# Kernel optimization log

Measured on AMD Instinct MI355X. Metric: run time of the kernel, lower is better.

The kernel has to match this reference:

```python
import jax, jax.numpy as jnp
import numpy as np

NUM_CLUSTERS = 16
CHANNELS = 256
UPDATE_RATE = 0.2
# channels % num_clusters == 0 -> all cluster capacities equal
_BASE = CHANNELS // NUM_CLUSTERS
_REM = CHANNELS % NUM_CLUSTERS
CLUSTER_SIZES = jnp.asarray([_BASE + 1] * _REM + [_BASE] * (NUM_CLUSTERS - _REM), dtype=jnp.int32)


def _cdist(a, b):
    # euclidean pairwise distance, batched over leading dims
    d2 = (jnp.sum(a * a, -1)[..., :, None]
          + jnp.sum(b * b, -1)[..., None, :]
          - 2.0 * (a @ jnp.swapaxes(b, -1, -2)))
    return jnp.sqrt(jnp.clip(d2, 0.0))


def _fps(D, k):
    # farthest point sampling given full [N,N] distance matrix
    start = jnp.argmax(D.sum(1))
    def step(min_d, _):
        far = jnp.argmax(min_d)
        return jnp.minimum(min_d, D[far]), far
    _, rest = jax.lax.scan(step, D[start], None, length=k - 1)
    return jnp.concatenate([start[None], rest])


def _capacity_assign(D, sizes):
    # greedy fixed-capacity assignment, sequential over channels
    order = jnp.argsort(D, axis=1)  # [C, K] cluster preference per channel
    def step(counts, row):
        avail = counts[row] < sizes[row]
        chosen = row[jnp.argmax(avail)]  # first available preference
        return counts.at[chosen].add(1), chosen
    _, assign = jax.lax.scan(step, jnp.zeros(sizes.shape[0], jnp.int32), order)
    return assign


def setup_inputs() -> dict:
    key = jax.random.key(0)
    k1, k2 = jax.random.split(key)
    features = jax.random.normal(k1, (8, CHANNELS, 64, 256), dtype=jnp.float32)
    pos_emb_batch = jax.random.normal(k2, (8, CHANNELS, 3), dtype=jnp.float32)
    return {"features": features, "pos_emb_batch": pos_emb_batch}


def reference(features, pos_emb_batch):
    b, c, nw, df = features.shape
    K = NUM_CLUSTERS
    pos = pos_emb_batch[0]                                   # [C, 3] (module's pos_emb buffer)
    # _initialize_centers: FPS over electrode positions
    centers = pos[_fps(_cdist(pos, pos), K)]                 # [K, 3]
    # _find_farthest_channels (euclidean): FPS over flattened features per batch
    ff = features.reshape(b, c, -1)
    Db = _cdist(ff, ff)                                      # [b, C, C]
    sel = jax.vmap(lambda D: _fps(D, K))(Db)                 # [b, K]
    # _cluster_euclidean_temp: nearest temp center per channel
    center_coords = pos_emb_batch[jnp.arange(b)[:, None], sel]      # [b, K, 3]
    temp_assign = jnp.argmin(_cdist(pos_emb_batch, center_coords), -1)  # [b, C]
    # per-cluster mean of positions over the whole batch
    flat_a = temp_assign.reshape(-1)
    flat_p = pos_emb_batch.reshape(-1, 3)
    sums = jax.ops.segment_sum(flat_p, flat_a, num_segments=K)
    cnts = jax.ops.segment_sum(jnp.ones(flat_a.shape, jnp.float32), flat_a, num_segments=K)
    avg = jnp.where(cnts[:, None] > 0, sums / jnp.maximum(cnts, 1.0)[:, None], 0.0)
    # match old centers to batch-average temp centers and EMA update
    matching = jnp.argmin(_cdist(centers, avg), axis=1)
    centers = (1.0 - UPDATE_RATE) * centers + UPDATE_RATE * avg[matching]
    # capacity-constrained final assignment
    return _capacity_assign(_cdist(pos, centers), CLUSTER_SIZES)
```

## Files before the change

kernel.cpp:

```cpp
#include <hip/hip_runtime.h>

#define NB 8
#define NC 256
#define DF 16384
#define KCL 16
#define SPLITS 8
#define KC (DF / SPLITS)
#define BK 32
#define ITERS (KC / BK)
#define NTILE 10

typedef _Float16 half8 __attribute__((ext_vector_type(8)));
typedef float floatx4 __attribute__((ext_vector_type(4)));

__device__ const int TItab[NTILE] = {0,0,0,0,1,1,1,2,2,3};
__device__ const int TJtab[NTILE] = {0,1,2,3,1,2,3,2,3,3};

__device__ __forceinline__ int argmax256(float v, float* sv, int* si) {
  int t = threadIdx.x;
  sv[t] = v; si[t] = t;
  __syncthreads();
  #pragma unroll
  for (int s = 128; s >= 1; s >>= 1) {
    if (t < s) {
      float a = sv[t], b = sv[t + s];
      int ia = si[t], ib = si[t + s];
      if (b > a || (b == a && ib < ia)) { sv[t] = b; si[t] = ib; }
    }
    __syncthreads();
  }
  int r = si[0];
  __syncthreads();
  return r;
}

__global__ __launch_bounds__(256) void k_pos_fps(const float* __restrict__ pe,
                                                 float* __restrict__ Dpos,
                                                 float* __restrict__ centers0) {
  __shared__ float px[NC], py[NC], pz[NC], pn[NC];
  __shared__ float sv[NC]; __shared__ int si[NC];
  __shared__ int fpsIdx[KCL];
  int t = threadIdx.x;
  float x = pe[t * 3 + 0], y = pe[t * 3 + 1], z = pe[t * 3 + 2];
  px[t] = x; py[t] = y; pz[t] = z;
  float n = x * x + y * y + z * z;
  pn[t] = n;
  __syncthreads();
  float rs = 0.f;
  for (int j = 0; j < NC; ++j) {
    float dot = x * px[j] + y * py[j] + z * pz[j];
    float d2 = n + pn[j] - 2.f * dot;
    float d = sqrtf(fmaxf(d2, 0.f));
    Dpos[j * NC + t] = d;
    rs += d;
  }
  __syncthreads();
  int start = argmax256(rs, sv, si);
  if (t == 0) fpsIdx[0] = start;
  float mind = Dpos[start * NC + t];
  for (int it = 1; it < KCL; ++it) {
    int far = argmax256(mind, sv, si);
    if (t == 0) fpsIdx[it] = far;
    mind = fminf(mind, Dpos[far * NC + t]);
  }
  __syncthreads();
  if (t < KCL) {
    int p = fpsIdx[t];
    centers0[t * 3 + 0] = px[p];
    centers0[t * 3 + 1] = py[p];
    centers0[t * 3 + 2] = pz[p];
  }
}

__global__ __launch_bounds__(256, 3) void k_gemm_mfma(const float* __restrict__ ff,
                                                      float* __restrict__ Pp) {
  __shared__ _Float16 Ah[64][40];
  __shared__ _Float16 Al[64][40];
  __shared__ _Float16 Bh[64][40];
  __shared__ _Float16 Bl[64][40];

  const int tid = threadIdx.x;
  const int tp = blockIdx.x;
  const int ti = TItab[tp], tj = TJtab[tp];
  const bool diag = (ti == tj);
  const int b = blockIdx.y, sp = blockIdx.z;
  const int wave = tid >> 6, lane = tid & 63;
  const int lrow = lane & 15, q = lane >> 4;

  const int sr = tid >> 2;
  const int sc = (tid & 3) * 8;
  const float* gA = ff + ((size_t)(b * NC + ti * 64 + sr)) * DF + sp * KC + sc;
  const float* gB = ff + ((size_t)(b * NC + tj * 64 + sr)) * DF + sp * KC + sc;

  floatx4 a1[4], a2[4], a3[4];
  #pragma unroll
  for (int j = 0; j < 4; ++j) { a1[j] = (floatx4)0.f; a2[j] = (floatx4)0.f; a3[j] = (floatx4)0.f; }

  float4 ra0 = *(const float4*)(gA), ra1 = *(const float4*)(gA + 4);
  float4 rb0 = make_float4(0.f, 0.f, 0.f, 0.f), rb1 = rb0;
  if (!diag) { rb0 = *(const float4*)(gB); rb1 = *(const float4*)(gB + 4); }
  gA += BK; gB += BK;

  for (int it = 0; it < ITERS; ++it) {
    float fa[8] = {ra0.x, ra0.y, ra0.z, ra0.w, ra1.x, ra1.y, ra1.z, ra1.w};
    half8 ah, al;
    #pragma unroll
    for (int e = 0; e < 8; ++e) {
      _Float16 h = (_Float16)fa[e];
      ah[e] = h;
      al[e] = (_Float16)(fa[e] - (float)h);
    }
    half8 bh, bl;
    if (!diag) {
      float fb[8] = {rb0.x, rb0.y, rb0.z, rb0.w, rb1.x, rb1.y, rb1.z, rb1.w};
      #pragma unroll
      for (int e = 0; e < 8; ++e) {
        _Float16 h = (_Float16)fb[e];
        bh[e] = h;
        bl[e] = (_Float16)(fb[e] - (float)h);
      }
    }
    __syncthreads();
    *(half8*)&Ah[sr][sc] = ah;
    *(half8*)&Al[sr][sc] = al;
    if (!diag) {
      *(half8*)&Bh[sr][sc] = bh;
      *(half8*)&Bl[sr][sc] = bl;
    }
    __syncthreads();
    if (it + 1 < ITERS) {
      ra0 = *(const float4*)(gA); ra1 = *(const float4*)(gA + 4);
      if (!diag) { rb0 = *(const float4*)(gB); rb1 = *(const float4*)(gB + 4); }
      gA += BK; gB += BK;
    }
    const _Float16* bhp = diag ? &Ah[0][0] : &Bh[0][0];
    const _Float16* blp = diag ? &Al[0][0] : &Bl[0][0];
    half8 af = *(const half8*)&Ah[wave * 16 + lrow][q * 8];
    half8 lf = *(const half8*)&Al[wave * 16 + lrow][q * 8];
    #pragma unroll
    for (int j = 0; j < 4; ++j) {
      half8 bhf = *(const half8*)(bhp + (j * 16 + lrow) * 40 + q * 8);
      half8 blf = *(const half8*)(blp + (j * 16 + lrow) * 40 + q * 8);
      a1[j] = __builtin_amdgcn_mfma_f32_16x16x32_f16(af, bhf, a1[j], 0, 0, 0);
      a2[j] = __builtin_amdgcn_mfma_f32_16x16x32_f16(af, blf, a2[j], 0, 0, 0);
      a3[j] = __builtin_amdgcn_mfma_f32_16x16x32_f16(lf, bhf, a3[j], 0, 0, 0);
    }
  }

  float* Pb = Pp + (size_t)(sp * NB + b) * NC * NC;
  int grow = ti * 64 + wave * 16 + q * 4;
  #pragma unroll
  for (int j = 0; j < 4; ++j) {
    int gcol = tj * 64 + j * 16 + lrow;
    float4 v;
    v.x = a1[j][0] + a2[j][0] + a3[j][0];
    v.y = a1[j][1] + a2[j][1] + a3[j][1];
    v.z = a1[j][2] + a2[j][2] + a3[j][2];
    v.w = a1[j][3] + a2[j][3] + a3[j][3];
    Pb[(size_t)(grow + 0) * NC + gcol] = v.x;
    Pb[(size_t)(grow + 1) * NC + gcol] = v.y;
    Pb[(size_t)(grow + 2) * NC + gcol] = v.z;
    Pb[(size_t)(grow + 3) * NC + gcol] = v.w;
    if (!diag) *(float4*)&Pb[(size_t)gcol * NC + grow] = v;
  }
}

__global__ __launch_bounds__(256) void k_diag(const float* __restrict__ Pp,
                                              float* __restrict__ dg) {
  int b = blockIdx.x, t = threadIdx.x;
  float s = 0.f;
  #pragma unroll
  for (int sp = 0; sp < SPLITS; ++sp)
    s += Pp[((size_t)(sp * NB + b) * NC + t) * NC + t];
  dg[b * NC + t] = s;
}

__global__ __launch_bounds__(256) void k_formD(const float* __restrict__ Pp,
                                               const float* __restrict__ dg,
                                               float* __restrict__ Db) {
  int i = blockIdx.x, b = blockIdx.y, j = threadIdx.x;
  float acc = 0.f;
  #pragma unroll
  for (int sp = 0; sp < SPLITS; ++sp)
    acc += Pp[((size_t)(sp * NB + b) * NC + i) * NC + j];
  float d2 = dg[b * NC + i] + dg[b * NC + j] - 2.f * acc;
  Db[((size_t)b * NC + i) * NC + j] = sqrtf(fmaxf(d2, 0.f));
}

__global__ __launch_bounds__(256) void k_fps_b(const float* __restrict__ Db,
                                               const float* __restrict__ pe,
                                               int* __restrict__ sel,
                                               float* __restrict__ ccoord) {
  int b = blockIdx.x, t = threadIdx.x;
  const float* D = Db + (size_t)b * NC * NC;
  __shared__ float sv[NC]; __shared__ int si[NC];
  __shared__ int fpsIdx[KCL];
  float rs = 0.f;
  for (int i = 0; i < NC; ++i) rs += D[i * NC + t];
  int start = argmax256(rs, sv, si);
  if (t == 0) fpsIdx[0] = start;
  float mind = D[start * NC + t];
  for (int it = 1; it < KCL; ++it) {
    int far = argmax256(mind, sv, si);
    if (t == 0) fpsIdx[it] = far;
    mind = fminf(mind, D[far * NC + t]);
  }
  __syncthreads();
  if (t < KCL) {
    int p = fpsIdx[t];
    sel[b * KCL + t] = p;
    ccoord[(b * KCL + t) * 3 + 0] = pe[(b * NC + p) * 3 + 0];
    ccoord[(b * KCL + t) * 3 + 1] = pe[(b * NC + p) * 3 + 1];
    ccoord[(b * KCL + t) * 3 + 2] = pe[(b * NC + p) * 3 + 2];
  }
}

__global__ __launch_bounds__(256) void k_final(const float* __restrict__ pe,
                                               const float* __restrict__ ccoord,
                                               const float* __restrict__ centers0,
                                               int* __restrict__ outp) {
  __shared__ float cc[NB * KCL * 3];
  __shared__ float cn[NB * KCL];
  __shared__ float sums[KCL][3];
  __shared__ int cnts[KCL];
  __shared__ float avg[KCL][3];
  __shared__ float an[KCL];
  __shared__ float c0[KCL * 3];
  __shared__ float c1x[KCL], c1y[KCL], c1z[KCL], c1n[KCL];
  __shared__ int order[NC][KCL];
  int t = threadIdx.x;
  for (int i = t; i < NB * KCL * 3; i += 256) cc[i] = ccoord[i];
  if (t < KCL * 3) c0[t] = centers0[t];
  if (t < KCL) { sums[t][0] = 0.f; sums[t][1] = 0.f; sums[t][2] = 0.f; cnts[t] = 0; }
  __syncthreads();
  if (t < NB * KCL) {
    float x = cc[t * 3], y = cc[t * 3 + 1], z = cc[t * 3 + 2];
    cn[t] = x * x + y * y + z * z;
  }
  __syncthreads();
  for (int b = 0; b < NB; ++b) {
    int p = b * NC + t;
    float x = pe[p * 3], y = pe[p * 3 + 1], z = pe[p * 3 + 2];
    float n = x * x + y * y + z * z;
    float best = 3.4e38f; int bi = 0;
    #pragma unroll
    for (int k = 0; k < KCL; ++k) {
      int c = b * KCL + k;
      float dot = x * cc[c * 3] + y * cc[c * 3 + 1] + z * cc[c * 3 + 2];
      float d2 = fmaxf(n + cn[c] - 2.f * dot, 0.f);
      if (d2 < best) { best = d2; bi = k; }
    }
    atomicAdd(&sums[bi][0], x);
    atomicAdd(&sums[bi][1], y);
    atomicAdd(&sums[bi][2], z);
    atomicAdd(&cnts[bi], 1);
  }
  __syncthreads();
  if (t < KCL) {
    float c = (float)cnts[t];
    float inv = 1.f / fmaxf(c, 1.f);
    float ax = (cnts[t] > 0) ? sums[t][0] * inv : 0.f;
    float ay = (cnts[t] > 0) ? sums[t][1] * inv : 0.f;
    float az = (cnts[t] > 0) ? sums[t][2] * inv : 0.f;
    avg[t][0] = ax; avg[t][1] = ay; avg[t][2] = az;
    an[t] = ax * ax + ay * ay + az * az;
  }
  __syncthreads();
  if (t < KCL) {
    float x = c0[t * 3], y = c0[t * 3 + 1], z = c0[t * 3 + 2];
    float n = x * x + y * y + z * z;
    float best = 3.4e38f; int bi = 0;
    #pragma unroll
    for (int j = 0; j < KCL; ++j) {
      float dot = x * avg[j][0] + y * avg[j][1] + z * avg[j][2];
      float d2 = fmaxf(n + an[j] - 2.f * dot, 0.f);
      if (d2 < best) { best = d2; bi = j; }
    }
    float nx = 0.8f * x + 0.2f * avg[bi][0];
    float ny = 0.8f * y + 0.2f * avg[bi][1];
    float nz = 0.8f * z + 0.2f * avg[bi][2];
    c1x[t] = nx; c1y[t] = ny; c1z[t] = nz;
    c1n[t] = nx * nx + ny * ny + nz * nz;
  }
  __syncthreads();
  {
    float x = pe[t * 3], y = pe[t * 3 + 1], z = pe[t * 3 + 2];
    float n = x * x + y * y + z * z;
    float v[KCL];
    #pragma unroll
    for (int k = 0; k < KCL; ++k) {
      float dot = x * c1x[k] + y * c1y[k] + z * c1z[k];
      v[k] = fmaxf(n + c1n[k] - 2.f * dot, 0.f);
    }
    bool used[KCL];
    #pragma unroll
    for (int k = 0; k < KCL; ++k) used[k] = false;
    for (int r = 0; r < KCL; ++r) {
      float best = 3.4e38f; int bi = 0;
      #pragma unroll
      for (int j = 0; j < KCL; ++j) {
        if (!used[j] && v[j] < best) { best = v[j]; bi = j; }
      }
      order[t][r] = bi;
      used[bi] = true;
    }
  }
  __syncthreads();
  if (t < 64) {
    int cnt = 0;
    int cur = (t < KCL) ? order[0][t] : 0;
    for (int i = 0; i < NC; ++i) {
      int nxt = (t < KCL && i + 1 < NC) ? order[i + 1][t] : 0;
      int ccur = __shfl(cnt, cur);
      bool avail = (t < KCL) && (ccur < 16);
      unsigned long long m = __ballot(avail);
      int chosen;
      if (m != 0ull) {
        int rank = __ffsll((unsigned long long)m) - 1;
        chosen = __shfl(cur, rank);
      } else {
        chosen = __shfl(cur, 0);
      }
      if (t == chosen) cnt++;
      if (t == 0) outp[i] = chosen;
      cur = nxt;
    }
  }
}

extern "C" void kernel_launch(void* const* d_in, const int* in_sizes, int n_in,
                              void* d_out, int out_size, void* d_ws, size_t ws_size,
                              hipStream_t stream) {
  (void)in_sizes; (void)n_in; (void)out_size; (void)ws_size;
  const float* features = (const float*)d_in[0];
  const float* pe = (const float*)d_in[1];
  char* ws = (char*)d_ws;
  float* Pp       = (float*)(ws);
  float* Db       = (float*)(ws + 16777216);
  float* Dpos     = (float*)(ws + 18874368);
  float* dg       = (float*)(ws + 19136512);
  float* centers0 = (float*)(ws + 19144704);
  int*   sel      = (int*)  (ws + 19145216);
  float* ccoord   = (float*)(ws + 19145728);
  int*   outp     = (int*)d_out;

  hipLaunchKernelGGL(k_pos_fps, dim3(1), dim3(256), 0, stream, pe, Dpos, centers0);
  hipLaunchKernelGGL(k_gemm_mfma, dim3(NTILE, NB, SPLITS), dim3(256), 0, stream, features, Pp);
  hipLaunchKernelGGL(k_diag, dim3(NB), dim3(256), 0, stream, Pp, dg);
  hipLaunchKernelGGL(k_formD, dim3(NC, NB), dim3(256), 0, stream, Pp, dg, Db);
  hipLaunchKernelGGL(k_fps_b, dim3(NB), dim3(256), 0, stream, Db, pe, sel, ccoord);
  hipLaunchKernelGGL(k_final, dim3(1), dim3(256), 0, stream, pe, ccoord, centers0, outp);
}
```

Before: 365.6 us.

## Fuse post-GEMM stages into one cooperative kernel and double split-K

Merges the diagonal, distance-forming, batched FPS and final assignment kernels into a single cooperative kernel that uses grid syncs in place of separate launches. Split-K for the Gram GEMM goes from 8 to 16 with a higher occupancy hint, which adds more blocks to the 10x8 tile grid. The position FPS now recomputes distances on the fly instead of writing and rereading a distance matrix. The trade-off is a doubled partial-product buffer (more traffic when reducing it), the cost of grid-wide syncs, and a dependence on cooperative-launch support and workspace size.

```diff
diff --git a/kernel.cpp b/kernel.cpp
--- a/kernel.cpp
+++ b/kernel.cpp
@@ -1,10 +1,13 @@
 #include <hip/hip_runtime.h>
+#include <hip/hip_cooperative_groups.h>
+
+namespace cg = cooperative_groups;
 
 #define NB 8
 #define NC 256
 #define DF 16384
 #define KCL 16
-#define SPLITS 8
+#define SPLITS 16
 #define KC (DF / SPLITS)
 #define BK 32
 #define ITERS (KC / BK)
@@ -34,9 +37,8 @@
   return r;
 }
 
-__global__ __launch_bounds__(256) void k_pos_fps(const float* __restrict__ pe,
-                                                 float* __restrict__ Dpos,
-                                                 float* __restrict__ centers0) {
+__global__ __launch_bounds__(256) void k_pre(const float* __restrict__ pe,
+                                             float* __restrict__ centers0) {
   __shared__ float px[NC], py[NC], pz[NC], pn[NC];
   __shared__ float sv[NC]; __shared__ int si[NC];
   __shared__ int fpsIdx[KCL];
@@ -50,18 +52,17 @@
   for (int j = 0; j < NC; ++j) {
     float dot = x * px[j] + y * py[j] + z * pz[j];
     float d2 = n + pn[j] - 2.f * dot;
-    float d = sqrtf(fmaxf(d2, 0.f));
-    Dpos[j * NC + t] = d;
-    rs += d;
-  }
-  __syncthreads();
+    rs += sqrtf(fmaxf(d2, 0.f));
+  }
   int start = argmax256(rs, sv, si);
   if (t == 0) fpsIdx[0] = start;
-  float mind = Dpos[start * NC + t];
+  float dot0 = x * px[start] + y * py[start] + z * pz[start];
+  float mind = sqrtf(fmaxf(n + pn[start] - 2.f * dot0, 0.f));
   for (int it = 1; it < KCL; ++it) {
     int far = argmax256(mind, sv, si);
     if (t == 0) fpsIdx[it] = far;
-    mind = fminf(mind, Dpos[far * NC + t]);
+    float dot = x * px[far] + y * py[far] + z * pz[far];
+    mind = fminf(mind, sqrtf(fmaxf(n + pn[far] - 2.f * dot, 0.f)));
   }
   __syncthreads();
   if (t < KCL) {
@@ -72,7 +73,7 @@
   }
 }
 
-__global__ __launch_bounds__(256, 3) void k_gemm_mfma(const float* __restrict__ ff,
+__global__ __launch_bounds__(256, 5) void k_gemm_mfma(const float* __restrict__ ff,
                                                       float* __restrict__ Pp) {
   __shared__ _Float16 Ah[64][40];
   __shared__ _Float16 Al[64][40];
@@ -165,165 +166,174 @@
   }
 }
 
-__global__ __launch_bounds__(256) void k_diag(const float* __restrict__ Pp,
-                                              float* __restrict__ dg) {
-  int b = blockIdx.x, t = threadIdx.x;
-  float s = 0.f;
-  #pragma unroll
-  for (int sp = 0; sp < SPLITS; ++sp)
-    s += Pp[((size_t)(sp * NB + b) * NC + t) * NC + t];
-  dg[b * NC + t] = s;
-}
-
-__global__ __launch_bounds__(256) void k_formD(const float* __restrict__ Pp,
-                                               const float* __restrict__ dg,
-                                               float* __restrict__ Db) {
-  int i = blockIdx.x, b = blockIdx.y, j = threadIdx.x;
-  float acc = 0.f;
-  #pragma unroll
-  for (int sp = 0; sp < SPLITS; ++sp)
-    acc += Pp[((size_t)(sp * NB + b) * NC + i) * NC + j];
-  float d2 = dg[b * NC + i] + dg[b * NC + j] - 2.f * acc;
-  Db[((size_t)b * NC + i) * NC + j] = sqrtf(fmaxf(d2, 0.f));
-}
-
-__global__ __launch_bounds__(256) void k_fps_b(const float* __restrict__ Db,
-                                               const float* __restrict__ pe,
-                                               int* __restrict__ sel,
-                                               float* __restrict__ ccoord) {
-  int b = blockIdx.x, t = threadIdx.x;
-  const float* D = Db + (size_t)b * NC * NC;
+__global__ __launch_bounds__(256) void k_coop(const float* __restrict__ pe,
+                                              const float* __restrict__ Pp,
+                                              float* __restrict__ dg,
+                                              float* __restrict__ Db,
+                                              const float* __restrict__ centers0,
+                                              float* __restrict__ ccoord,
+                                              int* __restrict__ outp) {
+  cg::grid_group grid = cg::this_grid();
   __shared__ float sv[NC]; __shared__ int si[NC];
   __shared__ int fpsIdx[KCL];
-  float rs = 0.f;
-  for (int i = 0; i < NC; ++i) rs += D[i * NC + t];
-  int start = argmax256(rs, sv, si);
-  if (t == 0) fpsIdx[0] = start;
-  float mind = D[start * NC + t];
-  for (int it = 1; it < KCL; ++it) {
-    int far = argmax256(mind, sv, si);
-    if (t == 0) fpsIdx[it] = far;
-    mind = fminf(mind, D[far * NC + t]);
-  }
-  __syncthreads();
-  if (t < KCL) {
-    int p = fpsIdx[t];
-    sel[b * KCL + t] = p;
-    ccoord[(b * KCL + t) * 3 + 0] = pe[(b * NC + p) * 3 + 0];
-    ccoord[(b * KCL + t) * 3 + 1] = pe[(b * NC + p) * 3 + 1];
-    ccoord[(b * KCL + t) * 3 + 2] = pe[(b * NC + p) * 3 + 2];
-  }
-}
-
-__global__ __launch_bounds__(256) void k_final(const float* __restrict__ pe,
-                                               const float* __restrict__ ccoord,
-                                               const float* __restrict__ centers0,
-                                               int* __restrict__ outp) {
-  __shared__ float cc[NB * KCL * 3];
-  __shared__ float cn[NB * KCL];
-  __shared__ float sums[KCL][3];
-  __shared__ int cnts[KCL];
-  __shared__ float avg[KCL][3];
-  __shared__ float an[KCL];
-  __shared__ float c0[KCL * 3];
-  __shared__ float c1x[KCL], c1y[KCL], c1z[KCL], c1n[KCL];
-  __shared__ int order[NC][KCL];
-  int t = threadIdx.x;
-  for (int i = t; i < NB * KCL * 3; i += 256) cc[i] = ccoord[i];
-  if (t < KCL * 3) c0[t] = centers0[t];
-  if (t < KCL) { sums[t][0] = 0.f; sums[t][1] = 0.f; sums[t][2] = 0.f; cnts[t] = 0; }
-  __syncthreads();
-  if (t < NB * KCL) {
-    float x = cc[t * 3], y = cc[t * 3 + 1], z = cc[t * 3 + 2];
-    cn[t] = x * x + y * y + z * z;
-  }
-  __syncthreads();
-  for (int b = 0; b < NB; ++b) {
-    int p = b * NC + t;
-    float x = pe[p * 3], y = pe[p * 3 + 1], z = pe[p * 3 + 2];
-    float n = x * x + y * y + z * z;
-    float best = 3.4e38f; int bi = 0;
+  const int t = threadIdx.x, g = blockIdx.x;
+
+  if (g < NB) {
+    float s = 0.f;
     #pragma unroll
-    for (int k = 0; k < KCL; ++k) {
-      int c = b * KCL + k;
-      float dot = x * cc[c * 3] + y * cc[c * 3 + 1] + z * cc[c * 3 + 2];
-      float d2 = fmaxf(n + cn[c] - 2.f * dot, 0.f);
-      if (d2 < best) { best = d2; bi = k; }
-    }
-    atomicAdd(&sums[bi][0], x);
-    atomicAdd(&sums[bi][1], y);
-    atomicAdd(&sums[bi][2], z);
-    atomicAdd(&cnts[bi], 1);
-  }
-  __syncthreads();
-  if (t < KCL) {
-    float c = (float)cnts[t];
-    float inv = 1.f / fmaxf(c, 1.f);
-    float ax = (cnts[t] > 0) ? sums[t][0] * inv : 0.f;
-    float ay = (cnts[t] > 0) ? sums[t][1] * inv : 0.f;
-    float az = (cnts[t] > 0) ? sums[t][2] * inv : 0.f;
-    avg[t][0] = ax; avg[t][1] = ay; avg[t][2] = az;
-    an[t] = ax * ax + ay * ay + az * az;
-  }
-  __syncthreads();
-  if (t < KCL) {
-    float x = c0[t * 3], y = c0[t * 3 + 1], z = c0[t * 3 + 2];
-    float n = x * x + y * y + z * z;
-    float best = 3.4e38f; int bi = 0;
-    #pragma unroll
-    for (int j = 0; j < KCL; ++j) {
-      float dot = x * avg[j][0] + y * avg[j][1] + z * avg[j][2];
-      float d2 = fmaxf(n + an[j] - 2.f * dot, 0.f);
-      if (d2 < best) { best = d2; bi = j; }
-    }
-    float nx = 0.8f * x + 0.2f * avg[bi][0];
-    float ny = 0.8f * y + 0.2f * avg[bi][1];
-    float nz = 0.8f * z + 0.2f * avg[bi][2];
-    c1x[t] = nx; c1y[t] = ny; c1z[t] = nz;
-    c1n[t] = nx * nx + ny * ny + nz * nz;
-  }
-  __syncthreads();
+    for (int sp = 0; sp < SPLITS; ++sp)
+      s += Pp[((size_t)(sp * NB + g) * NC + t) * NC + t];
+    dg[g * NC + t] = s;
+  }
+  __threadfence();
+  grid.sync();
+
   {
-    float x = pe[t * 3], y = pe[t * 3 + 1], z = pe[t * 3 + 2];
-    float n = x * x + y * y + z * z;
-    float v[KCL];
-    #pragma unroll
-    for (int k = 0; k < KCL; ++k) {
-      float dot = x * c1x[k] + y * c1y[k] + z * c1z[k];
-      v[k] = fmaxf(n + c1n[k] - 2.f * dot, 0.f);
-    }
-    bool used[KCL];
-    #pragma unroll
-    for (int k = 0; k < KCL; ++k) used[k] = false;
-    for (int r = 0; r < KCL; ++r) {
+    int b = g >> 5, i0 = (g & 31) * 8;
+    float dgj = dg[b * NC + t];
+    for (int ii = 0; ii < 8; ++ii) {
+      int i = i0 + ii;
+      float acc = 0.f;
+      #pragma unroll
+      for (int sp = 0; sp < SPLITS; ++sp)
+        acc += Pp[((size_t)(sp * NB + b) * NC + i) * NC + t];
+      float d2 = dg[b * NC + i] + dgj - 2.f * acc;
+      Db[((size_t)b * NC + i) * NC + t] = sqrtf(fmaxf(d2, 0.f));
+    }
+  }
+  __threadfence();
+  grid.sync();
+
+  if (g < NB) {
+    const float* D = Db + (size_t)g * NC * NC;
+    float rs = 0.f;
+    #pragma unroll 8
+    for (int i = 0; i < NC; ++i) rs += D[i * NC + t];
+    int start = argmax256(rs, sv, si);
+    if (t == 0) fpsIdx[0] = start;
+    float mind = D[start * NC + t];
+    for (int it = 1; it < KCL; ++it) {
+      int far = argmax256(mind, sv, si);
+      if (t == 0) fpsIdx[it] = far;
+      mind = fminf(mind, D[far * NC + t]);
+    }
+    __syncthreads();
+    if (t < KCL) {
+      int p = fpsIdx[t];
+      ccoord[(g * KCL + t) * 3 + 0] = pe[(g * NC + p) * 3 + 0];
+      ccoord[(g * KCL + t) * 3 + 1] = pe[(g * NC + p) * 3 + 1];
+      ccoord[(g * KCL + t) * 3 + 2] = pe[(g * NC + p) * 3 + 2];
+    }
+  }
+  __threadfence();
+  grid.sync();
+
+  if (g == 0) {
+    __shared__ float cc[NB * KCL * 3];
+    __shared__ float cn[NB * KCL];
+    __shared__ float sums[KCL][3];
+    __shared__ int cnts[KCL];
+    __shared__ float avg[KCL][3];
+    __shared__ float an[KCL];
+    __shared__ float c0[KCL * 3];
+    __shared__ float c1x[KCL], c1y[KCL], c1z[KCL], c1n[KCL];
+    __shared__ int order[NC][KCL];
+    for (int i = t; i < NB * KCL * 3; i += 256) cc[i] = ccoord[i];
+    if (t < KCL * 3) c0[t] = centers0[t];
+    if (t < KCL) { sums[t][0] = 0.f; sums[t][1] = 0.f; sums[t][2] = 0.f; cnts[t] = 0; }
+    __syncthreads();
+    if (t < NB * KCL) {
+      float x = cc[t * 3], y = cc[t * 3 + 1], z = cc[t * 3 + 2];
+      cn[t] = x * x + y * y + z * z;
+    }
+    __syncthreads();
+    for (int b = 0; b < NB; ++b) {
+      int p = b * NC + t;
+      float x = pe[p * 3], y = pe[p * 3 + 1], z = pe[p * 3 + 2];
+      float n = x * x + y * y + z * z;
       float best = 3.4e38f; int bi = 0;
       #pragma unroll
+      for (int k = 0; k < KCL; ++k) {
+        int c = b * KCL + k;
+        float dot = x * cc[c * 3] + y * cc[c * 3 + 1] + z * cc[c * 3 + 2];
+        float d2 = fmaxf(n + cn[c] - 2.f * dot, 0.f);
+        if (d2 < best) { best = d2; bi = k; }
+      }
+      atomicAdd(&sums[bi][0], x);
+      atomicAdd(&sums[bi][1], y);
+      atomicAdd(&sums[bi][2], z);
+      atomicAdd(&cnts[bi], 1);
+    }
+    __syncthreads();
+    if (t < KCL) {
+      float c = (float)cnts[t];
+      float inv = 1.f / fmaxf(c, 1.f);
+      float ax = (cnts[t] > 0) ? sums[t][0] * inv : 0.f;
+      float ay = (cnts[t] > 0) ? sums[t][1] * inv : 0.f;
+      float az = (cnts[t] > 0) ? sums[t][2] * inv : 0.f;
+      avg[t][0] = ax; avg[t][1] = ay; avg[t][2] = az;
+      an[t] = ax * ax + ay * ay + az * az;
+    }
+    __syncthreads();
+    if (t < KCL) {
+      float x = c0[t * 3], y = c0[t * 3 + 1], z = c0[t * 3 + 2];
+      float n = x * x + y * y + z * z;
+      float best = 3.4e38f; int bi = 0;
+      #pragma unroll
       for (int j = 0; j < KCL; ++j) {
-        if (!used[j] && v[j] < best) { best = v[j]; bi = j; }
-      }
-      order[t][r] = bi;
-      used[bi] = true;
-    }
-  }
-  __syncthreads();
-  if (t < 64) {
-    int cnt = 0;
-    int cur = (t < KCL) ? order[0][t] : 0;
-    for (int i = 0; i < NC; ++i) {
-      int nxt = (t < KCL && i + 1 < NC) ? order[i + 1][t] : 0;
-      int ccur = __shfl(cnt, cur);
-      bool avail = (t < KCL) && (ccur < 16);
-      unsigned long long m = __ballot(avail);
-      int chosen;
-      if (m != 0ull) {
-        int rank = __ffsll((unsigned long long)m) - 1;
-        chosen = __shfl(cur, rank);
-      } else {
-        chosen = __shfl(cur, 0);
-      }
-      if (t == chosen) cnt++;
-      if (t == 0) outp[i] = chosen;
-      cur = nxt;
+        float dot = x * avg[j][0] + y * avg[j][1] + z * avg[j][2];
+        float d2 = fmaxf(n + an[j] - 2.f * dot, 0.f);
+        if (d2 < best) { best = d2; bi = j; }
+      }
+      float nx = 0.8f * x + 0.2f * avg[bi][0];
+      float ny = 0.8f * y + 0.2f * avg[bi][1];
+      float nz = 0.8f * z + 0.2f * avg[bi][2];
+      c1x[t] = nx; c1y[t] = ny; c1z[t] = nz;
+      c1n[t] = nx * nx + ny * ny + nz * nz;
+    }
+    __syncthreads();
+    {
+      float x = pe[t * 3], y = pe[t * 3 + 1], z = pe[t * 3 + 2];
+      float n = x * x + y * y + z * z;
+      float v[KCL];
+      #pragma unroll
+      for (int k = 0; k < KCL; ++k) {
+        float dot = x * c1x[k] + y * c1y[k] + z * c1z[k];
+        v[k] = fmaxf(n + c1n[k] - 2.f * dot, 0.f);
+      }
+      bool used[KCL];
+      #pragma unroll
+      for (int k = 0; k < KCL; ++k) used[k] = false;
+      for (int r = 0; r < KCL; ++r) {
+        float best = 3.4e38f; int bi = 0;
+        #pragma unroll
+        for (int j = 0; j < KCL; ++j) {
+          if (!used[j] && v[j] < best) { best = v[j]; bi = j; }
+        }
+        order[t][r] = bi;
+        used[bi] = true;
+      }
+    }
+    __syncthreads();
+    if (t < 64) {
+      int cnt = 0;
+      int cur = (t < KCL) ? order[0][t] : 0;
+      for (int i = 0; i < NC; ++i) {
+        int nxt = (t < KCL && i + 1 < NC) ? order[i + 1][t] : 0;
+        int ccur = __shfl(cnt, cur);
+        bool avail = (t < KCL) && (ccur < 16);
+        unsigned long long m = __ballot(avail);
+        int chosen;
+        if (m != 0ull) {
+          int rank = __ffsll((unsigned long long)m) - 1;
+          chosen = __shfl(cur, rank);
+        } else {
+          chosen = __shfl(cur, 0);
+        }
+        if (t == chosen) cnt++;
+        if (t == 0) outp[i] = chosen;
+        cur = nxt;
+      }
     }
   }
 }
@@ -336,18 +346,16 @@
   const float* pe = (const float*)d_in[1];
   char* ws = (char*)d_ws;
   float* Pp       = (float*)(ws);
-  float* Db       = (float*)(ws + 16777216);
-  float* Dpos     = (float*)(ws + 18874368);
-  float* dg       = (float*)(ws + 19136512);
-  float* centers0 = (float*)(ws + 19144704);
-  int*   sel      = (int*)  (ws + 19145216);
-  float* ccoord   = (float*)(ws + 19145728);
+  float* Db       = (float*)(ws + 33554432);
+  float* dg       = (float*)(ws + 35651584);
+  float* centers0 = (float*)(ws + 35659776);
+  float* ccoord   = (float*)(ws + 35660288);
   int*   outp     = (int*)d_out;
 
-  hipLaunchKernelGGL(k_pos_fps, dim3(1), dim3(256), 0, stream, pe, Dpos, centers0);
+  hipLaunchKernelGGL(k_pre, dim3(1), dim3(256), 0, stream, pe, centers0);
   hipLaunchKernelGGL(k_gemm_mfma, dim3(NTILE, NB, SPLITS), dim3(256), 0, stream, features, Pp);
-  hipLaunchKernelGGL(k_diag, dim3(NB), dim3(256), 0, stream, Pp, dg);
-  hipLaunchKernelGGL(k_formD, dim3(NC, NB), dim3(256), 0, stream, Pp, dg, Db);
-  hipLaunchKernelGGL(k_fps_b, dim3(NB), dim3(256), 0, stream, Db, pe, sel, ccoord);
-  hipLaunchKernelGGL(k_final, dim3(1), dim3(256), 0, stream, pe, ccoord, centers0, outp);
-}
+
+  void* args[] = {(void*)&pe, (void*)&Pp, (void*)&dg, (void*)&Db,
+                  (void*)&centers0, (void*)&ccoord, (void*)&outp};
+  hipLaunchCooperativeKernel((void*)k_coop, dim3(256), dim3(256), args, 0, stream);
+}
```

After: 524.4 us. 43.4% more time.

## Use 128x128 GEMM tiles with more K-splits and fuse diag/row-sum into formD

Applied to the files above, without the earlier changes.

The Gram GEMM now uses 128x128 output tiles (3 symmetric tiles) with 512-thread blocks and 16 K-splits. This cuts redundant feature reads of the symmetric block pairs while keeping the grid large enough to fill the GPU. The diagonal kernel is folded into formD, which also accumulates per-column distance sums with atomics, so the FPS kernel no longer rescans the whole distance matrix. The position FPS recomputes distances on the fly instead of writing and reading a distance matrix. The costs are a larger partial-product buffer to reduce and non-deterministic atomic float summation order.

```diff
diff --git a/kernel.cpp b/kernel.cpp
--- a/kernel.cpp
+++ b/kernel.cpp
@@ -4,17 +4,17 @@
 #define NC 256
 #define DF 16384
 #define KCL 16
-#define SPLITS 8
+#define SPLITS 16
 #define KC (DF / SPLITS)
 #define BK 32
 #define ITERS (KC / BK)
-#define NTILE 10
+#define NTILE 3
 
 typedef _Float16 half8 __attribute__((ext_vector_type(8)));
 typedef float floatx4 __attribute__((ext_vector_type(4)));
 
-__device__ const int TItab[NTILE] = {0,0,0,0,1,1,1,2,2,3};
-__device__ const int TJtab[NTILE] = {0,1,2,3,1,2,3,2,3,3};
+__device__ const int TItab[NTILE] = {0,0,1};
+__device__ const int TJtab[NTILE] = {0,1,1};
 
 __device__ __forceinline__ int argmax256(float v, float* sv, int* si) {
   int t = threadIdx.x;
@@ -34,34 +34,34 @@
   return r;
 }
 
-__global__ __launch_bounds__(256) void k_pos_fps(const float* __restrict__ pe,
-                                                 float* __restrict__ Dpos,
-                                                 float* __restrict__ centers0) {
+__global__ __launch_bounds__(256) void k_pre(const float* __restrict__ pe,
+                                             float* __restrict__ centers0,
+                                             float* __restrict__ rs) {
   __shared__ float px[NC], py[NC], pz[NC], pn[NC];
   __shared__ float sv[NC]; __shared__ int si[NC];
   __shared__ int fpsIdx[KCL];
   int t = threadIdx.x;
+  for (int i = t; i < NB * NC; i += 256) rs[i] = 0.f;
   float x = pe[t * 3 + 0], y = pe[t * 3 + 1], z = pe[t * 3 + 2];
   px[t] = x; py[t] = y; pz[t] = z;
   float n = x * x + y * y + z * z;
   pn[t] = n;
   __syncthreads();
-  float rs = 0.f;
+  float rsum = 0.f;
   for (int j = 0; j < NC; ++j) {
     float dot = x * px[j] + y * py[j] + z * pz[j];
     float d2 = n + pn[j] - 2.f * dot;
-    float d = sqrtf(fmaxf(d2, 0.f));
-    Dpos[j * NC + t] = d;
-    rs += d;
-  }
-  __syncthreads();
-  int start = argmax256(rs, sv, si);
+    rsum += sqrtf(fmaxf(d2, 0.f));
+  }
+  int start = argmax256(rsum, sv, si);
   if (t == 0) fpsIdx[0] = start;
-  float mind = Dpos[start * NC + t];
+  float dot0 = x * px[start] + y * py[start] + z * pz[start];
+  float mind = sqrtf(fmaxf(n + pn[start] - 2.f * dot0, 0.f));
   for (int it = 1; it < KCL; ++it) {
     int far = argmax256(mind, sv, si);
     if (t == 0) fpsIdx[it] = far;
-    mind = fminf(mind, Dpos[far * NC + t]);
+    float dot = x * px[far] + y * py[far] + z * pz[far];
+    mind = fminf(mind, sqrtf(fmaxf(n + pn[far] - 2.f * dot, 0.f)));
   }
   __syncthreads();
   if (t < KCL) {
@@ -72,29 +72,31 @@
   }
 }
 
-__global__ __launch_bounds__(256, 3) void k_gemm_mfma(const float* __restrict__ ff,
+__global__ __launch_bounds__(512, 2) void k_gemm_mfma(const float* __restrict__ ff,
                                                       float* __restrict__ Pp) {
-  __shared__ _Float16 Ah[64][40];
-  __shared__ _Float16 Al[64][40];
-  __shared__ _Float16 Bh[64][40];
-  __shared__ _Float16 Bl[64][40];
+  __shared__ _Float16 Ah[128][40];
+  __shared__ _Float16 Al[128][40];
+  __shared__ _Float16 Bh[128][40];
+  __shared__ _Float16 Bl[128][40];
 
   const int tid = threadIdx.x;
-  const int tp = blockIdx.x;
-  const int ti = TItab[tp], tj = TJtab[tp];
+  const int ti = TItab[blockIdx.x], tj = TJtab[blockIdx.x];
   const bool diag = (ti == tj);
   const int b = blockIdx.y, sp = blockIdx.z;
   const int wave = tid >> 6, lane = tid & 63;
+  const int wr = wave >> 1, wc = wave & 1;
   const int lrow = lane & 15, q = lane >> 4;
 
   const int sr = tid >> 2;
   const int sc = (tid & 3) * 8;
-  const float* gA = ff + ((size_t)(b * NC + ti * 64 + sr)) * DF + sp * KC + sc;
-  const float* gB = ff + ((size_t)(b * NC + tj * 64 + sr)) * DF + sp * KC + sc;
-
-  floatx4 a1[4], a2[4], a3[4];
+  const float* gA = ff + ((size_t)(b * NC + ti * 128 + sr)) * DF + sp * KC + sc;
+  const float* gB = ff + ((size_t)(b * NC + tj * 128 + sr)) * DF + sp * KC + sc;
+
+  floatx4 a1[2][4], a2[2][4], a3[2][4];
   #pragma unroll
-  for (int j = 0; j < 4; ++j) { a1[j] = (floatx4)0.f; a2[j] = (floatx4)0.f; a3[j] = (floatx4)0.f; }
+  for (int i = 0; i < 2; ++i)
+    #pragma unroll
+    for (int j = 0; j < 4; ++j) { a1[i][j] = (floatx4)0.f; a2[i][j] = (floatx4)0.f; a3[i][j] = (floatx4)0.f; }
 
   float4 ra0 = *(const float4*)(gA), ra1 = *(const float4*)(gA + 4);
   float4 rb0 = make_float4(0.f, 0.f, 0.f, 0.f), rb1 = rb0;
@@ -135,69 +137,82 @@
     }
     const _Float16* bhp = diag ? &Ah[0][0] : &Bh[0][0];
     const _Float16* blp = diag ? &Al[0][0] : &Bl[0][0];
-    half8 af = *(const half8*)&Ah[wave * 16 + lrow][q * 8];
-    half8 lf = *(const half8*)&Al[wave * 16 + lrow][q * 8];
+    half8 af[2], lf[2];
+    #pragma unroll
+    for (int i = 0; i < 2; ++i) {
+      af[i] = *(const half8*)&Ah[wr * 32 + i * 16 + lrow][q * 8];
+      lf[i] = *(const half8*)&Al[wr * 32 + i * 16 + lrow][q * 8];
+    }
     #pragma unroll
     for (int j = 0; j < 4; ++j) {
-      half8 bhf = *(const half8*)(bhp + (j * 16 + lrow) * 40 + q * 8);
-      half8 blf = *(const half8*)(blp + (j * 16 + lrow) * 40 + q * 8);
-      a1[j] = __builtin_amdgcn_mfma_f32_16x16x32_f16(af, bhf, a1[j], 0, 0, 0);
-      a2[j] = __builtin_amdgcn_mfma_f32_16x16x32_f16(af, blf, a2[j], 0, 0, 0);
-      a3[j] = __builtin_amdgcn_mfma_f32_16x16x32_f16(lf, bhf, a3[j], 0, 0, 0);
+      half8 bhf = *(const half8*)(bhp + (wc * 64 + j * 16 + lrow) * 40 + q * 8);
+      half8 blf = *(const half8*)(blp + (wc * 64 + j * 16 + lrow) * 40 + q * 8);
+      #pragma unroll
+      for (int i = 0; i < 2; ++i) {
+        a1[i][j] = __builtin_amdgcn_mfma_f32_16x16x32_f16(af[i], bhf, a1[i][j], 0, 0, 0);
+        a2[i][j] = __builtin_amdgcn_mfma_f32_16x16x32_f16(af[i], blf, a2[i][j], 0, 0, 0);
+        a3[i][j] = __builtin_amdgcn_mfma_f32_16x16x32_f16(lf[i], bhf, a3[i][j], 0, 0, 0);
+      }
     }
   }
 
   float* Pb = Pp + (size_t)(sp * NB + b) * NC * NC;
-  int grow = ti * 64 + wave * 16 + q * 4;
   #pragma unroll
-  for (int j = 0; j < 4; ++j) {
-    int gcol = tj * 64 + j * 16 + lrow;
-    float4 v;
-    v.x = a1[j][0] + a2[j][0] + a3[j][0];
-    v.y = a1[j][1] + a2[j][1] + a3[j][1];
-    v.z = a1[j][2] + a2[j][2] + a3[j][2];
-    v.w = a1[j][3] + a2[j][3] + a3[j][3];
-    Pb[(size_t)(grow + 0) * NC + gcol] = v.x;
-    Pb[(size_t)(grow + 1) * NC + gcol] = v.y;
-    Pb[(size_t)(grow + 2) * NC + gcol] = v.z;
-    Pb[(size_t)(grow + 3) * NC + gcol] = v.w;
-    if (!diag) *(float4*)&Pb[(size_t)gcol * NC + grow] = v;
-  }
-}
-
-__global__ __launch_bounds__(256) void k_diag(const float* __restrict__ Pp,
-                                              float* __restrict__ dg) {
-  int b = blockIdx.x, t = threadIdx.x;
+  for (int i = 0; i < 2; ++i) {
+    int grow = ti * 128 + wr * 32 + i * 16 + q * 4;
+    #pragma unroll
+    for (int j = 0; j < 4; ++j) {
+      int gcol = tj * 128 + wc * 64 + j * 16 + lrow;
+      float4 v;
+      v.x = a1[i][j][0] + a2[i][j][0] + a3[i][j][0];
+      v.y = a1[i][j][1] + a2[i][j][1] + a3[i][j][1];
+      v.z = a1[i][j][2] + a2[i][j][2] + a3[i][j][2];
+      v.w = a1[i][j][3] + a2[i][j][3] + a3[i][j][3];
+      Pb[(size_t)(grow + 0) * NC + gcol] = v.x;
+      Pb[(size_t)(grow + 1) * NC + gcol] = v.y;
+      Pb[(size_t)(grow + 2) * NC + gcol] = v.z;
+      Pb[(size_t)(grow + 3) * NC + gcol] = v.w;
+      if (!diag) *(float4*)&Pb[(size_t)gcol * NC + grow] = v;
+    }
+  }
+}
+
+__global__ __launch_bounds__(256) void k_formD(const float* __restrict__ Pp,
+                                               float* __restrict__ Db,
+                                               float* __restrict__ rs) {
+  __shared__ float dg_s[NC];
+  const int t = threadIdx.x;
+  const int b = blockIdx.x >> 5, i0 = (blockIdx.x & 31) * 8;
   float s = 0.f;
   #pragma unroll
   for (int sp = 0; sp < SPLITS; ++sp)
     s += Pp[((size_t)(sp * NB + b) * NC + t) * NC + t];
-  dg[b * NC + t] = s;
-}
-
-__global__ __launch_bounds__(256) void k_formD(const float* __restrict__ Pp,
-                                               const float* __restrict__ dg,
-                                               float* __restrict__ Db) {
-  int i = blockIdx.x, b = blockIdx.y, j = threadIdx.x;
-  float acc = 0.f;
-  #pragma unroll
-  for (int sp = 0; sp < SPLITS; ++sp)
-    acc += Pp[((size_t)(sp * NB + b) * NC + i) * NC + j];
-  float d2 = dg[b * NC + i] + dg[b * NC + j] - 2.f * acc;
-  Db[((size_t)b * NC + i) * NC + j] = sqrtf(fmaxf(d2, 0.f));
+  dg_s[t] = s;
+  __syncthreads();
+  float colsum = 0.f;
+  for (int ii = 0; ii < 8; ++ii) {
+    int i = i0 + ii;
+    float acc = 0.f;
+    #pragma unroll
+    for (int sp = 0; sp < SPLITS; ++sp)
+      acc += Pp[((size_t)(sp * NB + b) * NC + i) * NC + t];
+    float d2 = dg_s[i] + dg_s[t] - 2.f * acc;
+    float d = sqrtf(fmaxf(d2, 0.f));
+    Db[((size_t)b * NC + i) * NC + t] = d;
+    colsum += d;
+  }
+  atomicAdd(&rs[b * NC + t], colsum);
 }
 
 __global__ __launch_bounds__(256) void k_fps_b(const float* __restrict__ Db,
+                                               const float* __restrict__ rs,
                                                const float* __restrict__ pe,
-                                               int* __restrict__ sel,
                                                float* __restrict__ ccoord) {
   int b = blockIdx.x, t = threadIdx.x;
   const float* D = Db + (size_t)b * NC * NC;
   __shared__ float sv[NC]; __shared__ int si[NC];
   __shared__ int fpsIdx[KCL];
-  float rs = 0.f;
-  for (int i = 0; i < NC; ++i) rs += D[i * NC + t];
-  int start = argmax256(rs, sv, si);
+  int start = argmax256(rs[b * NC + t], sv, si);
   if (t == 0) fpsIdx[0] = start;
   float mind = D[start * NC + t];
   for (int it = 1; it < KCL; ++it) {
@@ -208,7 +223,6 @@
   __syncthreads();
   if (t < KCL) {
     int p = fpsIdx[t];
-    sel[b * KCL + t] = p;
     ccoord[(b * KCL + t) * 3 + 0] = pe[(b * NC + p) * 3 + 0];
     ccoord[(b * KCL + t) * 3 + 1] = pe[(b * NC + p) * 3 + 1];
     ccoord[(b * KCL + t) * 3 + 2] = pe[(b * NC + p) * 3 + 2];
@@ -336,18 +350,15 @@
   const float* pe = (const float*)d_in[1];
   char* ws = (char*)d_ws;
   float* Pp       = (float*)(ws);
-  float* Db       = (float*)(ws + 16777216);
-  float* Dpos     = (float*)(ws + 18874368);
-  float* dg       = (float*)(ws + 19136512);
-  float* centers0 = (float*)(ws + 19144704);
-  int*   sel      = (int*)  (ws + 19145216);
-  float* ccoord   = (float*)(ws + 19145728);
+  float* Db       = (float*)(ws + 33554432);
+  float* rs       = (float*)(ws + 35651584);
+  float* centers0 = (float*)(ws + 35659776);
+  float* ccoord   = (float*)(ws + 35660288);
   int*   outp     = (int*)d_out;
 
-  hipLaunchKernelGGL(k_pos_fps, dim3(1), dim3(256), 0, stream, pe, Dpos, centers0);
-  hipLaunchKernelGGL(k_gemm_mfma, dim3(NTILE, NB, SPLITS), dim3(256), 0, stream, features, Pp);
-  hipLaunchKernelGGL(k_diag, dim3(NB), dim3(256), 0, stream, Pp, dg);
-  hipLaunchKernelGGL(k_formD, dim3(NC, NB), dim3(256), 0, stream, Pp, dg, Db);
-  hipLaunchKernelGGL(k_fps_b, dim3(NB), dim3(256), 0, stream, Db, pe, sel, ccoord);
+  hipLaunchKernelGGL(k_pre, dim3(1), dim3(256), 0, stream, pe, centers0, rs);
+  hipLaunchKernelGGL(k_gemm_mfma, dim3(NTILE, NB, SPLITS), dim3(512), 0, stream, features, Pp);
+  hipLaunchKernelGGL(k_formD, dim3(256), dim3(256), 0, stream, Pp, Db, rs);
+  hipLaunchKernelGGL(k_fps_b, dim3(NB), dim3(256), 0, stream, Db, rs, pe, ccoord);
   hipLaunchKernelGGL(k_final, dim3(1), dim3(256), 0, stream, pe, ccoord, centers0, outp);
 }
```

Result: no change. 366.4 us (+0.2%).
